# Kernel optimization log

Hardware: AMD Instinct MI355X
Metric: run time of the kernel (lower is better)

## Reference

```python
import jax, jax.numpy as jnp
import numpy as np

HIDDEN_DIM = 1024
NUM_HEADS = 16
HEAD_DIM = HIDDEN_DIM // NUM_HEADS
ROPE_BASE = 10000.0


def setup_inputs() -> dict:
    key = jax.random.key(0)
    kx, kq, kk, kv, ko = jax.random.split(key, 5)
    B, S = 2, 2048
    scale = 1.0 / np.sqrt(HIDDEN_DIM)
    x = jax.random.normal(kx, (B, S, HIDDEN_DIM), dtype=jnp.float32)
    Wq = jax.random.normal(kq, (HIDDEN_DIM, HIDDEN_DIM), dtype=jnp.float32) * scale
    Wk = jax.random.normal(kk, (HIDDEN_DIM, HIDDEN_DIM), dtype=jnp.float32) * scale
    Wv = jax.random.normal(kv, (HIDDEN_DIM, HIDDEN_DIM), dtype=jnp.float32) * scale
    Wo = jax.random.normal(ko, (HIDDEN_DIM, HIDDEN_DIM), dtype=jnp.float32) * scale
    return {"x": x, "Wq": Wq, "Wk": Wk, "Wv": Wv, "Wo": Wo}


def _apply_rope(t, positions):
    # t: (B, S, H, D), positions: (B, S)
    half = HEAD_DIM // 2
    inv_freq = 1.0 / (ROPE_BASE ** (jnp.arange(0, half, dtype=jnp.float32) * 2.0 / HEAD_DIM))
    freqs = positions[..., None].astype(jnp.float32) * inv_freq  # (B, S, D/2)
    emb = jnp.concatenate([freqs, freqs], axis=-1)  # (B, S, D)
    cos = jnp.cos(emb)[:, :, None, :]
    sin = jnp.sin(emb)[:, :, None, :]
    t1, t2 = t[..., :half], t[..., half:]
    rot = jnp.concatenate([-t2, t1], axis=-1)
    return t * cos + rot * sin


def reference(x, Wq, Wk, Wv, Wo):
    B, S, _ = x.shape
    H, D = NUM_HEADS, HEAD_DIM
    q = (x @ Wq.T).reshape(B, S, H, D)
    k = (x @ Wk.T).reshape(B, S, H, D)
    v = (x @ Wv.T).reshape(B, S, H, D)
    positions = jnp.broadcast_to(jnp.arange(S)[None, :], (B, S))
    q = _apply_rope(q, positions)
    k = _apply_rope(k, positions)
    # SDPA (non-causal, no mask): scores (B, H, S, S)
    scale = 1.0 / np.sqrt(D)
    scores = jnp.einsum('bqhd,bkhd->bhqk', q, k) * scale
    probs = jax.nn.softmax(scores, axis=-1)
    out = jnp.einsum('bhqk,bkhd->bqhd', probs, v).reshape(B, S, H * D)
    return out @ Wo.T
```

## Files before the change

kernel.cpp:

```cpp
#include <hip/hip_runtime.h>


typedef unsigned short u16;
typedef __bf16 bf16x8 __attribute__((ext_vector_type(8)));
typedef float  f32x4  __attribute__((ext_vector_type(4)));
typedef u16    u16x8  __attribute__((ext_vector_type(8)));
typedef u16    u16x4  __attribute__((ext_vector_type(4)));

#define HID 1024
#define SEQ 2048
#define NH  16
#define HD  64

#if __has_builtin(__builtin_amdgcn_exp2f)
#define EXP2F(x) __builtin_amdgcn_exp2f(x)
#else
#define EXP2F(x) exp2f(x)
#endif

__device__ __forceinline__ float bf2f(u16 u) { return __uint_as_float(((unsigned)u) << 16); }
__device__ __forceinline__ u16 f2bf(float f) {
  union { __bf16 h; u16 u; } c;
  c.h = (__bf16)f;
  return c.u;
}
__device__ __forceinline__ void gl_lds16(const void* g, void* l) {
  __builtin_amdgcn_global_load_lds((const __attribute__((address_space(1))) void*)g,
                                   (__attribute__((address_space(3))) void*)l, 16, 0, 0);
}
__device__ __forceinline__ void stage_f32(const float* __restrict__ src, u16* dst) {
  float4 f0 = *(const float4*)src;
  float4 f1 = *(const float4*)(src + 4);
  u16x8 o;
  o[0] = f2bf(f0.x); o[1] = f2bf(f0.y); o[2] = f2bf(f0.z); o[3] = f2bf(f0.w);
  o[4] = f2bf(f1.x); o[5] = f2bf(f1.y); o[6] = f2bf(f1.z); o[7] = f2bf(f1.w);
  *(u16x8*)dst = o;
}
__device__ __forceinline__ int swz(int c, int r) { return c ^ (r & 7); }

__global__ void cvt_pre(const float* __restrict__ x,  const float* __restrict__ Wq,
                        const float* __restrict__ Wk, const float* __restrict__ Wv,
                        u16* __restrict__ xb, u16* __restrict__ Wqb,
                        u16* __restrict__ Wkb, u16* __restrict__ Wvb) {
  const int z = blockIdx.y;
  const float* src; u16* dst; int nchunk;
  switch (z) {
    case 0:  src = x;  dst = xb;  nchunk = 524288; break;
    case 1:  src = Wq; dst = Wqb; nchunk = 131072; break;
    case 2:  src = Wk; dst = Wkb; nchunk = 131072; break;
    default: src = Wv; dst = Wvb; nchunk = 131072; break;
  }
  const int i = blockIdx.x * 256 + threadIdx.x;
  if (i >= nchunk) return;
  stage_f32(src + (size_t)i * 8, dst + (size_t)i * 8);
}
__global__ void cvt_wo(const float* __restrict__ Wo, u16* __restrict__ Wob) {
  const int i = blockIdx.x * 256 + threadIdx.x;
  stage_f32(Wo + (size_t)i * 8, Wob + (size_t)i * 8);
}

__device__ __forceinline__ void gemm_mainloop(const u16* __restrict__ Aptr,
                                              const u16* __restrict__ Bptr,
                                              u16* a_lds, u16* b_lds,
                                              int m0, int n0, f32x4 (&acc)[4][4]) {
  const int tid  = threadIdx.x;
  const int w    = tid >> 6;
  const int lane = tid & 63;
  const int quad = lane >> 4, l15 = lane & 15;
  const int wm = (w >> 1) * 64, wn = (w & 1) * 64;
  const int srow = lane >> 3, sc = lane & 7;

  for (int k0 = 0; k0 < HID; k0 += 64) {
#pragma unroll
    for (int i = 0; i < 4; ++i) {
      const int seg = w * 4 + i;
      const int r   = seg * 8 + srow;
      const int col = k0 + swz(sc, srow) * 8;
      gl_lds16(Aptr + (size_t)(m0 + r) * HID + col, a_lds + seg * 512);
      gl_lds16(Bptr + (size_t)(n0 + r) * HID + col, b_lds + seg * 512);
    }
    __syncthreads();
#pragma unroll
    for (int kf = 0; kf < 2; ++kf) {
      bf16x8 af[4], bfr[4];
#pragma unroll
      for (int mt = 0; mt < 4; ++mt)
        af[mt] = *(const bf16x8*)&a_lds[(wm + mt * 16 + l15) * 64 + swz(kf * 4 + quad, l15) * 8];
#pragma unroll
      for (int nt = 0; nt < 4; ++nt)
        bfr[nt] = *(const bf16x8*)&b_lds[(wn + nt * 16 + l15) * 64 + swz(kf * 4 + quad, l15) * 8];
#pragma unroll
      for (int mt = 0; mt < 4; ++mt)
#pragma unroll
        for (int nt = 0; nt < 4; ++nt)
          acc[mt][nt] = __builtin_amdgcn_mfma_f32_16x16x32_bf16(af[mt], bfr[nt], acc[mt][nt], 0, 0, 0);
    }
    __syncthreads();
  }
}

__device__ __forceinline__ void gemm64_mainloop(const u16* __restrict__ Aptr,
                                                const u16* __restrict__ Bptr,
                                                u16* a_lds, u16* b_lds,
                                                int m0, int n0, f32x4 (&acc)[2][4]) {
  const int tid  = threadIdx.x;
  const int w    = tid >> 6;
  const int lane = tid & 63;
  const int quad = lane >> 4, l15 = lane & 15;
  const int wm = (w >> 1) * 32, wn = (w & 1) * 64;
  const int srow = lane >> 3, sc = lane & 7;

  for (int k0 = 0; k0 < HID; k0 += 64) {
#pragma unroll
    for (int i = 0; i < 2; ++i) {
      const int seg = w * 2 + i, r = seg * 8 + srow;
      gl_lds16(Aptr + (size_t)(m0 + r) * HID + k0 + swz(sc, srow) * 8, a_lds + seg * 512);
    }
#pragma unroll
    for (int i = 0; i < 4; ++i) {
      const int seg = w * 4 + i, r = seg * 8 + srow;
      gl_lds16(Bptr + (size_t)(n0 + r) * HID + k0 + swz(sc, srow) * 8, b_lds + seg * 512);
    }
    __syncthreads();
#pragma unroll
    for (int kf = 0; kf < 2; ++kf) {
      bf16x8 af[2], bfr[4];
#pragma unroll
      for (int mt = 0; mt < 2; ++mt)
        af[mt] = *(const bf16x8*)&a_lds[(wm + mt * 16 + l15) * 64 + swz(kf * 4 + quad, l15) * 8];
#pragma unroll
      for (int nt = 0; nt < 4; ++nt)
        bfr[nt] = *(const bf16x8*)&b_lds[(wn + nt * 16 + l15) * 64 + swz(kf * 4 + quad, l15) * 8];
#pragma unroll
      for (int mt = 0; mt < 2; ++mt)
#pragma unroll
        for (int nt = 0; nt < 4; ++nt)
          acc[mt][nt] = __builtin_amdgcn_mfma_f32_16x16x32_bf16(af[mt], bfr[nt], acc[mt][nt], 0, 0, 0);
    }
    __syncthreads();
  }
}

#define QS_LOG2E 0.18033688011112042f
__global__ __launch_bounds__(256, 2) void qkv_gemm(const u16* __restrict__ xb,
                                                   const u16* __restrict__ Wqb,
                                                   const u16* __restrict__ Wkb,
                                                   const u16* __restrict__ Wvb,
                                                   u16* __restrict__ q, u16* __restrict__ k,
                                                   u16* __restrict__ vT) {
  __shared__ __align__(16) u16 a_lds[128 * 64];
  __shared__ __align__(16) u16 b_lds[128 * 64];
  const int z = blockIdx.z;
  const u16* W = (z == 0) ? Wqb : (z == 1) ? Wkb : Wvb;

  f32x4 acc[4][4];
#pragma unroll
  for (int i = 0; i < 4; ++i)
#pragma unroll
    for (int j = 0; j < 4; ++j) acc[i][j] = (f32x4){0.f, 0.f, 0.f, 0.f};

  const int m0 = blockIdx.y * 128, n0 = blockIdx.x * 128;
  gemm_mainloop(xb, W, a_lds, b_lds, m0, n0, acc);

  const int tid = threadIdx.x, w = tid >> 6, lane = tid & 63;
  const int quad = lane >> 4, l15 = lane & 15;
  const int wm = (w >> 1) * 64, wn = (w & 1) * 64;

  if (z != 2) {
    float fr[2];
    fr[0] = __expf(-(float)(l15)      * 0.2878231366242557f);
    fr[1] = __expf(-(float)(16 + l15) * 0.2878231366242557f);
    const float qs = (z == 0) ? QS_LOG2E : 1.f;
#pragma unroll
    for (int mt = 0; mt < 4; ++mt)
#pragma unroll
      for (int r = 0; r < 4; ++r) {
        const int s = (m0 + wm + mt * 16 + quad * 4 + r) & 2047;
#pragma unroll
        for (int p = 0; p < 2; ++p) {
          float c, sn;
          __sincosf((float)s * fr[p], &sn, &c);
          const float t1 = acc[mt][p][r], t2 = acc[mt][p + 2][r];
          acc[mt][p][r]     = (t1 * c - t2 * sn) * qs;
          acc[mt][p + 2][r] = (t2 * c + t1 * sn) * qs;
        }
      }
    u16* dst = (z == 0) ? q : k;
#pragma unroll
    for (int mt = 0; mt < 4; ++mt)
#pragma unroll
      for (int nt = 0; nt < 4; ++nt) {
        const int col = n0 + wn + nt * 16 + l15;
        const int h = col >> 6, d = col & 63;
#pragma unroll
        for (int r = 0; r < 4; ++r) {
          const int row = m0 + wm + mt * 16 + quad * 4 + r;
          const int bh  = (row >> 11) * NH + h;
          dst[((size_t)bh * SEQ + (row & 2047)) * HD + d] = f2bf(acc[mt][nt][r]);
        }
      }
  } else {
#pragma unroll
    for (int mt = 0; mt < 4; ++mt) {
      const int rowbase = m0 + wm + mt * 16 + quad * 4;
      const int b = rowbase >> 11, s0 = rowbase & 2047;
#pragma unroll
      for (int nt = 0; nt < 4; ++nt) {
        const int col = n0 + wn + nt * 16 + l15;
        const int h = col >> 6, d = col & 63;
        u16x4 o;
#pragma unroll
        for (int r = 0; r < 4; ++r) o[r] = f2bf(acc[mt][nt][r]);
        *(u16x4*)&vT[((size_t)(b * NH + h) * HD + d) * SEQ + s0] = o;
      }
    }
  }
}

__global__ __launch_bounds__(512, 4) void flash(const u16* __restrict__ q,
                                                const u16* __restrict__ k,
                                                const u16* __restrict__ vT,
                                                u16* __restrict__ o0, u16* __restrict__ o1,
                                                float* __restrict__ L0, float* __restrict__ L1) {
  __shared__ __align__(16) u16 ktl[2 * 4096];
  __shared__ __align__(16) u16 vtl[2 * 4096];
  __shared__ __align__(16) u16 pl[8 * 16 * 64];

  const int tid = threadIdx.x, w = tid >> 6, lane = tid & 63;
  const int quad = lane >> 4, l15 = lane & 15;
  const int srow = lane >> 3, sc = lane & 7;
  const int bh = blockIdx.y;
  const int q0 = blockIdx.x * 256;
  const int z  = blockIdx.z;
  u16*   odst = z ? o1 : o0;
  float* Ldst = z ? L1 : L0;

  bf16x8 qa[2][2];
#pragma unroll
  for (int qh = 0; qh < 2; ++qh) {
    const u16* qrow = q + ((size_t)bh * SEQ + q0 + w * 32 + qh * 16 + l15) * HD + quad * 8;
    qa[qh][0] = *(const bf16x8*)qrow;
    qa[qh][1] = *(const bf16x8*)(qrow + 32);
  }

  const f32x4 zero4 = (f32x4){0.f, 0.f, 0.f, 0.f};
  f32x4 oacc[2][4];
#pragma unroll
  for (int qh = 0; qh < 2; ++qh)
#pragma unroll
    for (int i = 0; i < 4; ++i) oacc[qh][i] = zero4;
  float L[2] = {0.f, 0.f};

  const u16* kbase = k  + (size_t)bh * SEQ * HD + (size_t)z * 1024 * HD;
  const u16* vtb   = vT + (size_t)bh * HD * SEQ + (size_t)z * 1024;

  {
    const int seg = w, r = seg * 8 + srow, col = swz(sc, srow) * 8;
    gl_lds16(kbase + (size_t)r * HD + col,  &ktl[seg * 512]);
    gl_lds16(vtb   + (size_t)r * SEQ + col, &vtl[seg * 512]);
  }
  __syncthreads();

  for (int t = 0; t < 16; ++t) {
    const int t0 = t * 64, buf = t & 1;
    if (t < 15) {
      const int seg = w, r = seg * 8 + srow, col = swz(sc, srow) * 8;
      gl_lds16(kbase + (size_t)(t0 + 64 + r) * HD + col, &ktl[(buf ^ 1) * 4096 + seg * 512]);
      gl_lds16(vtb   + (size_t)r * SEQ + t0 + 64 + col,  &vtl[(buf ^ 1) * 4096 + seg * 512]);
    }

    bf16x8 kfr[2][4], bvf[2][4];
#pragma unroll
    for (int kf = 0; kf < 2; ++kf)
#pragma unroll
      for (int nt = 0; nt < 4; ++nt) {
        kfr[kf][nt] = *(const bf16x8*)&ktl[buf * 4096 + (nt * 16 + l15) * 64 + swz(kf * 4 + quad, l15) * 8];
        bvf[kf][nt] = *(const bf16x8*)&vtl[buf * 4096 + (nt * 16 + l15) * 64 + swz(kf * 4 + quad, l15) * 8];
      }

    u16* pw = &pl[w * 16 * 64];
#pragma unroll
    for (int qh = 0; qh < 2; ++qh) {
      f32x4 sv[4];
#pragma unroll
      for (int nt = 0; nt < 4; ++nt) {
        sv[nt] = __builtin_amdgcn_mfma_f32_16x16x32_bf16(kfr[0][nt], qa[qh][0], zero4, 0, 0, 0);
        sv[nt] = __builtin_amdgcn_mfma_f32_16x16x32_bf16(kfr[1][nt], qa[qh][1], sv[nt], 0, 0, 0);
      }
#pragma unroll
      for (int nt = 0; nt < 4; ++nt) {
        u16x4 pk;
#pragma unroll
        for (int r = 0; r < 4; ++r) {
          const float pv = EXP2F(sv[nt][r]);
          L[qh] += pv;
          pk[r] = f2bf(pv);
        }
        const int cw = 2 * nt + (quad >> 1);
        *(u16x4*)&pw[l15 * 64 + swz(cw, l15) * 8 + 4 * (quad & 1)] = pk;
      }
#pragma unroll
      for (int kf = 0; kf < 2; ++kf) {
        bf16x8 ap = *(const bf16x8*)&pw[l15 * 64 + swz(kf * 4 + quad, l15) * 8];
#pragma unroll
        for (int dt = 0; dt < 4; ++dt)
          oacc[qh][dt] = __builtin_amdgcn_mfma_f32_16x16x32_bf16(ap, bvf[kf][dt], oacc[qh][dt], 0, 0, 0);
      }
    }
    __syncthreads();
  }

#pragma unroll
  for (int qh = 0; qh < 2; ++qh) {
    L[qh] += __shfl_xor(L[qh], 16, 64);
    L[qh] += __shfl_xor(L[qh], 32, 64);
    if (quad == 0) Ldst[(size_t)bh * SEQ + q0 + w * 32 + qh * 16 + l15] = L[qh];
  }

  const int b = bh >> 4, h = bh & 15;
#pragma unroll
  for (int qh = 0; qh < 2; ++qh)
#pragma unroll
    for (int r = 0; r < 4; ++r) {
      const int row = b * SEQ + q0 + w * 32 + qh * 16 + quad * 4 + r;
#pragma unroll
      for (int dt = 0; dt < 4; ++dt)
        odst[(size_t)row * HID + h * HD + dt * 16 + l15] = f2bf(oacc[qh][dt][r]);
    }
}

__global__ void combine(const u16* __restrict__ o1, const float* __restrict__ L0,
                        const float* __restrict__ L1, u16* __restrict__ attn) {
  const size_t base = ((size_t)blockIdx.x * 256 + threadIdx.x) * 8;
  const int row = (int)(base >> 10);
  const int h   = ((int)base & 1023) >> 6;
  const int bh  = (row >> 11) * NH + h;
  const int s   = row & 2047;
  const float inv = 1.f / (L0[(size_t)bh * SEQ + s] + L1[(size_t)bh * SEQ + s]);
  u16x8 a = *(const u16x8*)&attn[base];
  u16x8 b = *(const u16x8*)&o1[base];
  u16x8 o;
#pragma unroll
  for (int j = 0; j < 8; ++j) o[j] = f2bf((bf2f(a[j]) + bf2f(b[j])) * inv);
  *(u16x8*)&attn[base] = o;
}

__global__ __launch_bounds__(256, 4) void out_gemm(const u16* __restrict__ attn,
                                                   const u16* __restrict__ Wob,
                                                   float* __restrict__ out) {
  __shared__ __align__(16) u16 a_lds[64 * 64];
  __shared__ __align__(16) u16 b_lds[128 * 64];
  f32x4 acc[2][4];
#pragma unroll
  for (int i = 0; i < 2; ++i)
#pragma unroll
    for (int j = 0; j < 4; ++j) acc[i][j] = (f32x4){0.f, 0.f, 0.f, 0.f};

  const int m0 = blockIdx.y * 64, n0 = blockIdx.x * 128;
  gemm64_mainloop(attn, Wob, a_lds, b_lds, m0, n0, acc);

  const int tid = threadIdx.x, w = tid >> 6, lane = tid & 63;
  const int quad = lane >> 4, l15 = lane & 15;
  const int wm = (w >> 1) * 32, wn = (w & 1) * 64;
#pragma unroll
  for (int mt = 0; mt < 2; ++mt)
#pragma unroll
    for (int nt = 0; nt < 4; ++nt) {
      const int col = n0 + wn + nt * 16 + l15;
#pragma unroll
      for (int r = 0; r < 4; ++r) {
        const int row = m0 + wm + mt * 16 + quad * 4 + r;
        out[(size_t)row * HID + col] = acc[mt][nt][r];
      }
    }
}

extern "C" void kernel_launch(void* const* d_in, const int* in_sizes, int n_in,
                              void* d_out, int out_size, void* d_ws, size_t ws_size,
                              hipStream_t stream) {
  const float* x  = (const float*)d_in[0];
  const float* Wq = (const float*)d_in[1];
  const float* Wk = (const float*)d_in[2];
  const float* Wv = (const float*)d_in[3];
  const float* Wo = (const float*)d_in[4];
  float* out = (float*)d_out;

  char* os = (char*)d_out;
  u16* Wqb = (u16*)(os);
  u16* Wkb = (u16*)(os + (2u << 20));
  u16* Wvb = (u16*)(os + (4u << 20));
  u16* xb  = (u16*)(os + (6u << 20));
  u16*   o1 = (u16*)(os);
  float* L0 = (float*)(os + (8u << 20));
  float* L1 = (float*)(os + (8u << 20) + (256u << 10));

  char* ws = (char*)d_ws;
  u16* q    = (u16*)(ws);
  u16* Wob  = (u16*)(ws);
  u16* k    = (u16*)(ws + (8u << 20));
  u16* vT   = (u16*)(ws + (16u << 20));
  u16* attn = (u16*)(ws + (24u << 20));

  cvt_pre<<<dim3(2048, 4), 256, 0, stream>>>(x, Wq, Wk, Wv, xb, Wqb, Wkb, Wvb);
  qkv_gemm<<<dim3(8, 32, 3), 256, 0, stream>>>(xb, Wqb, Wkb, Wvb, q, k, vT);
  flash<<<dim3(8, 32, 2), 512, 0, stream>>>(q, k, vT, attn, o1, L0, L1);
  cvt_wo<<<dim3(512), 256, 0, stream>>>(Wo, Wob);
  combine<<<dim3(2048), 256, 0, stream>>>(o1, L0, L1, attn);
  out_gemm<<<dim3(8, 64), 256, 0, stream>>>(attn, Wob, out);
}
```

Before: 181.3 us.

## Drop KV split in flash attention, triple-buffer K/V loads, fuse normalization

The flash kernel no longer splits the key range across two grid slices. Each block now iterates all 32 key tiles with a three-stage LDS ring buffer, explicit vmcnt waits and a single barrier per tile. Softmax normalization by the row sum is applied in the epilogue, so the separate combine kernel and its partial-output and L buffers go away. The cost is half as many blocks (256) for the 256 CUs and a launch bound lowered to 2 waves, which may leave the machine underfilled and lengthen each block's serial loop.

```diff
diff --git a/kernel.cpp b/kernel.cpp
--- a/kernel.cpp
+++ b/kernel.cpp
@@ -217,13 +217,12 @@
   }
 }
 
-__global__ __launch_bounds__(512, 4) void flash(const u16* __restrict__ q,
+__global__ __launch_bounds__(512, 2) void flash(const u16* __restrict__ q,
                                                 const u16* __restrict__ k,
                                                 const u16* __restrict__ vT,
-                                                u16* __restrict__ o0, u16* __restrict__ o1,
-                                                float* __restrict__ L0, float* __restrict__ L1) {
-  __shared__ __align__(16) u16 ktl[2 * 4096];
-  __shared__ __align__(16) u16 vtl[2 * 4096];
+                                                u16* __restrict__ attn) {
+  __shared__ __align__(16) u16 ktl[3 * 4096];
+  __shared__ __align__(16) u16 vtl[3 * 4096];
   __shared__ __align__(16) u16 pl[8 * 16 * 64];
 
   const int tid = threadIdx.x, w = tid >> 6, lane = tid & 63;
@@ -231,9 +230,9 @@
   const int srow = lane >> 3, sc = lane & 7;
   const int bh = blockIdx.y;
   const int q0 = blockIdx.x * 256;
-  const int z  = blockIdx.z;
-  u16*   odst = z ? o1 : o0;
-  float* Ldst = z ? L1 : L0;
+
+  const u16* kbase = k  + (size_t)bh * SEQ * HD;
+  const u16* vtb   = vT + (size_t)bh * HD * SEQ;
 
   bf16x8 qa[2][2];
 #pragma unroll
@@ -243,6 +242,19 @@
     qa[qh][1] = *(const bf16x8*)(qrow + 32);
   }
 
+  const int r8 = w * 8 + srow;
+  const int colsw = swz(sc, srow) * 8;
+#define ISSUE(T, B) do {                                                              \
+    gl_lds16(kbase + (size_t)((T) * 64 + r8) * HD + colsw, &ktl[(B) * 4096 + w * 512]); \
+    gl_lds16(vtb + (size_t)r8 * SEQ + (T) * 64 + colsw,    &vtl[(B) * 4096 + w * 512]); \
+  } while (0)
+
+  ISSUE(0, 0);
+  ISSUE(1, 1);
+  asm volatile("s_waitcnt vmcnt(2)" ::: "memory");
+  __builtin_amdgcn_s_barrier();
+  __builtin_amdgcn_sched_barrier(0);
+
   const f32x4 zero4 = (f32x4){0.f, 0.f, 0.f, 0.f};
   f32x4 oacc[2][4];
 #pragma unroll
@@ -251,33 +263,17 @@
     for (int i = 0; i < 4; ++i) oacc[qh][i] = zero4;
   float L[2] = {0.f, 0.f};
 
-  const u16* kbase = k  + (size_t)bh * SEQ * HD + (size_t)z * 1024 * HD;
-  const u16* vtb   = vT + (size_t)bh * HD * SEQ + (size_t)z * 1024;
-
-  {
-    const int seg = w, r = seg * 8 + srow, col = swz(sc, srow) * 8;
-    gl_lds16(kbase + (size_t)r * HD + col,  &ktl[seg * 512]);
-    gl_lds16(vtb   + (size_t)r * SEQ + col, &vtl[seg * 512]);
-  }
-  __syncthreads();
-
-  for (int t = 0; t < 16; ++t) {
-    const int t0 = t * 64, buf = t & 1;
-    if (t < 15) {
-      const int seg = w, r = seg * 8 + srow, col = swz(sc, srow) * 8;
-      gl_lds16(kbase + (size_t)(t0 + 64 + r) * HD + col, &ktl[(buf ^ 1) * 4096 + seg * 512]);
-      gl_lds16(vtb   + (size_t)r * SEQ + t0 + 64 + col,  &vtl[(buf ^ 1) * 4096 + seg * 512]);
-    }
-
+  auto compute = [&](int cb) {
+    const u16* kc = &ktl[cb * 4096];
+    const u16* vc = &vtl[cb * 4096];
     bf16x8 kfr[2][4], bvf[2][4];
 #pragma unroll
     for (int kf = 0; kf < 2; ++kf)
 #pragma unroll
       for (int nt = 0; nt < 4; ++nt) {
-        kfr[kf][nt] = *(const bf16x8*)&ktl[buf * 4096 + (nt * 16 + l15) * 64 + swz(kf * 4 + quad, l15) * 8];
-        bvf[kf][nt] = *(const bf16x8*)&vtl[buf * 4096 + (nt * 16 + l15) * 64 + swz(kf * 4 + quad, l15) * 8];
-      }
-
+        kfr[kf][nt] = *(const bf16x8*)&kc[(nt * 16 + l15) * 64 + swz(kf * 4 + quad, l15) * 8];
+        bvf[kf][nt] = *(const bf16x8*)&vc[(nt * 16 + l15) * 64 + swz(kf * 4 + quad, l15) * 8];
+      }
     u16* pw = &pl[w * 16 * 64];
 #pragma unroll
     for (int qh = 0; qh < 2; ++qh) {
@@ -307,42 +303,43 @@
           oacc[qh][dt] = __builtin_amdgcn_mfma_f32_16x16x32_bf16(ap, bvf[kf][dt], oacc[qh][dt], 0, 0, 0);
       }
     }
-    __syncthreads();
-  }
-
+  };
+
+  int cur = 0, nxt = 2;
+  for (int t = 0; t < 30; ++t) {
+    ISSUE(t + 2, nxt);
+    __builtin_amdgcn_sched_barrier(0);
+    compute(cur);
+    asm volatile("s_waitcnt vmcnt(2)" ::: "memory");
+    __builtin_amdgcn_s_barrier();
+    __builtin_amdgcn_sched_barrier(0);
+    cur = (cur == 2) ? 0 : cur + 1;
+    nxt = (nxt == 2) ? 0 : nxt + 1;
+  }
+  compute(0);
+  asm volatile("s_waitcnt vmcnt(0)" ::: "memory");
+  __builtin_amdgcn_s_barrier();
+  __builtin_amdgcn_sched_barrier(0);
+  compute(1);
+#undef ISSUE
+
+  const int b = bh >> 4, h = bh & 15;
 #pragma unroll
   for (int qh = 0; qh < 2; ++qh) {
-    L[qh] += __shfl_xor(L[qh], 16, 64);
-    L[qh] += __shfl_xor(L[qh], 32, 64);
-    if (quad == 0) Ldst[(size_t)bh * SEQ + q0 + w * 32 + qh * 16 + l15] = L[qh];
-  }
-
-  const int b = bh >> 4, h = bh & 15;
-#pragma unroll
-  for (int qh = 0; qh < 2; ++qh)
+    float Lf = L[qh];
+    Lf += __shfl_xor(Lf, 16, 64);
+    Lf += __shfl_xor(Lf, 32, 64);
+    float inv[4];
+#pragma unroll
+    for (int r = 0; r < 4; ++r) inv[r] = 1.f / __shfl(Lf, quad * 4 + r, 64);
 #pragma unroll
     for (int r = 0; r < 4; ++r) {
       const int row = b * SEQ + q0 + w * 32 + qh * 16 + quad * 4 + r;
 #pragma unroll
       for (int dt = 0; dt < 4; ++dt)
-        odst[(size_t)row * HID + h * HD + dt * 16 + l15] = f2bf(oacc[qh][dt][r]);
-    }
-}
-
-__global__ void combine(const u16* __restrict__ o1, const float* __restrict__ L0,
-                        const float* __restrict__ L1, u16* __restrict__ attn) {
-  const size_t base = ((size_t)blockIdx.x * 256 + threadIdx.x) * 8;
-  const int row = (int)(base >> 10);
-  const int h   = ((int)base & 1023) >> 6;
-  const int bh  = (row >> 11) * NH + h;
-  const int s   = row & 2047;
-  const float inv = 1.f / (L0[(size_t)bh * SEQ + s] + L1[(size_t)bh * SEQ + s]);
-  u16x8 a = *(const u16x8*)&attn[base];
-  u16x8 b = *(const u16x8*)&o1[base];
-  u16x8 o;
-#pragma unroll
-  for (int j = 0; j < 8; ++j) o[j] = f2bf((bf2f(a[j]) + bf2f(b[j])) * inv);
-  *(u16x8*)&attn[base] = o;
+        attn[(size_t)row * HID + h * HD + dt * 16 + l15] = f2bf(oacc[qh][dt][r] * inv[r]);
+    }
+  }
 }
 
 __global__ __launch_bounds__(256, 4) void out_gemm(const u16* __restrict__ attn,
@@ -390,9 +387,6 @@
   u16* Wkb = (u16*)(os + (2u << 20));
   u16* Wvb = (u16*)(os + (4u << 20));
   u16* xb  = (u16*)(os + (6u << 20));
-  u16*   o1 = (u16*)(os);
-  float* L0 = (float*)(os + (8u << 20));
-  float* L1 = (float*)(os + (8u << 20) + (256u << 10));
 
   char* ws = (char*)d_ws;
   u16* q    = (u16*)(ws);
@@ -403,8 +397,7 @@
 
   cvt_pre<<<dim3(2048, 4), 256, 0, stream>>>(x, Wq, Wk, Wv, xb, Wqb, Wkb, Wvb);
   qkv_gemm<<<dim3(8, 32, 3), 256, 0, stream>>>(xb, Wqb, Wkb, Wvb, q, k, vT);
-  flash<<<dim3(8, 32, 2), 512, 0, stream>>>(q, k, vT, attn, o1, L0, L1);
+  flash<<<dim3(8, 32), 512, 0, stream>>>(q, k, vT, attn);
   cvt_wo<<<dim3(512), 256, 0, stream>>>(Wo, Wob);
-  combine<<<dim3(2048), 256, 0, stream>>>(o1, L0, L1, attn);
   out_gemm<<<dim3(8, 64), 256, 0, stream>>>(attn, Wob, out);
 }
```

After: 180.3 us. No clear change (-0.6%).
